# Kernel optimization log

Hardware: AMD Instinct MI355X
Metric: run time of the kernel (lower is better)

## Reference

```python
import jax, jax.numpy as jnp
import numpy as np

NEG = -1e30  # log-space 'zero'


def setup_inputs() -> dict:
    B, T, C, L = 64, 2000, 128, 200  # C = num_classes + 1, blank = C - 1
    key = jax.random.key(0)
    k1, k2, k3 = jax.random.split(key, 3)
    y_pred = jax.random.normal(k1, (B, T, C), dtype=jnp.float32)
    label_lengths = jax.random.randint(k2, (B,), L // 2, L + 1).astype(jnp.int32)
    labels = jax.random.randint(k3, (B, L), 0, C - 1).astype(jnp.int32)  # never blank
    # pad with -1 beyond each label length (matches tf sparse construction)
    valid = jnp.arange(L)[None, :] < label_lengths[:, None]
    y_true = jnp.where(valid, labels, -1).astype(jnp.int32)
    # train_step fills input_lengths with the full time dimension
    input_lengths = jnp.full((B,), T, dtype=jnp.int32)
    return {"y_pred": y_pred, "y_true": y_true,
            "input_lengths": input_lengths, "label_lengths": label_lengths}


def _lse3(a, b, c):
    m = jnp.maximum(jnp.maximum(a, b), c)
    return m + jnp.log(jnp.exp(a - m) + jnp.exp(b - m) + jnp.exp(c - m))


def _ctc_loss(y_pred, y_true, input_lengths, label_lengths):
    B, T, C = y_pred.shape
    blank = C - 1  # blank_index=-1 in tf.nn.ctc_loss
    logp = jax.nn.log_softmax(y_pred, axis=-1)          # [B,T,C]
    Lmax = y_true.shape[1]
    S = 2 * Lmax + 1                                     # extended label lattice
    lab = jnp.where(y_true < 0, 0, y_true).astype(jnp.int32)
    # extended labels: blank, l0, blank, l1, ..., blank
    ext = jnp.full((B, S), blank, jnp.int32).at[:, 1::2].set(lab)
    ext_m2 = jnp.concatenate([jnp.full((B, 2), blank, jnp.int32), ext[:, :-2]], axis=1)
    can_skip = (ext != blank) & (ext != ext_m2)          # [B,S]

    logp_t = jnp.transpose(logp, (1, 0, 2))              # [T,B,C]
    lp0 = jnp.take_along_axis(logp_t[0], ext, axis=1)    # [B,S]
    alpha = jnp.full((B, S), NEG, jnp.float32)
    alpha = alpha.at[:, 0].set(lp0[:, 0]).at[:, 1].set(lp0[:, 1])

    def step(alpha, xs):
        lp, t = xs                                       # lp: [B,C]
        lp_ext = jnp.take_along_axis(lp, ext, axis=1)    # [B,S]
        a1 = jnp.concatenate([jnp.full((B, 1), NEG, jnp.float32), alpha[:, :-1]], axis=1)
        a2 = jnp.concatenate([jnp.full((B, 2), NEG, jnp.float32), alpha[:, :-2]], axis=1)
        a2 = jnp.where(can_skip, a2, NEG)
        new = _lse3(alpha, a1, a2) + lp_ext
        new = jnp.where(t < input_lengths[:, None], new, alpha)  # freeze past seq end
        return new, None

    alpha, _ = jax.lax.scan(step, alpha, (logp_t[1:], jnp.arange(1, T)))

    s_end = (2 * label_lengths).astype(jnp.int32)        # [B]
    a_last = jnp.take_along_axis(alpha, s_end[:, None], axis=1)[:, 0]
    a_prev = jnp.take_along_axis(alpha, jnp.maximum(s_end - 1, 0)[:, None], axis=1)[:, 0]
    m = jnp.maximum(a_last, a_prev)
    ll = m + jnp.log(jnp.exp(a_last - m) + jnp.exp(a_prev - m))
    return -ll                                           # per-example loss [B]


def reference(y_pred, y_true, input_lengths, label_lengths):
    return _ctc_loss(y_pred, y_true, input_lengths, label_lengths)
```

## Files before the change

kernel.cpp:

```cpp
#include <hip/hip_runtime.h>
#include <hip/hip_fp16.h>


#define LOG2E 1.44269504088896340736f
#define LN2F  0.69314718055994530942f

namespace {

constexpr int Bc = 64, Tc = 2000, Cc = 128, Lmaxc = 200;
constexpr int NPAIR = Tc / 2;
constexpr int PAIRB = 1024;
constexpr int BLANKB = 8192;
constexpr size_t SB = (size_t)NPAIR * PAIRB + BLANKB;
constexpr int CHP = 16;
constexpr int CHB = CHP * PAIRB;

typedef const __attribute__((address_space(1))) void* gas_ptr;
typedef __attribute__((address_space(3))) void* las_ptr;

__device__ __forceinline__ float dpp_shr1_f(float x) {
  return __int_as_float(
      __builtin_amdgcn_update_dpp(0, __float_as_int(x), 0x138, 0xF, 0xF, true));
}
__device__ __forceinline__ int dpp_shr1_i(int x) {
  return __builtin_amdgcn_update_dpp(0, x, 0x138, 0xF, 0xF, true);
}
template <int CTRL>
__device__ __forceinline__ float dpp_add(float v) {
  return v + __int_as_float(
      __builtin_amdgcn_update_dpp(0, __float_as_int(v), CTRL, 0xF, 0xF, true));
}
__device__ __forceinline__ float wave_sum_bcast(float v) {
  v = dpp_add<0x111>(v);
  v = dpp_add<0x112>(v);
  v = dpp_add<0x114>(v);
  v = dpp_add<0x118>(v);
  v = dpp_add<0x142>(v);
  v = dpp_add<0x143>(v);
  return __int_as_float(__builtin_amdgcn_readlane(__float_as_int(v), 63));
}

__global__ __launch_bounds__(256) void pack_kernel(
    const float* __restrict__ y, const int* __restrict__ y_true,
    char* __restrict__ W) {
  const int b = blockIdx.y;
  const int wv = threadIdx.x >> 6, lane = threadIdx.x & 63;
  const int t = blockIdx.x * 4 + wv;
  const int* labs = y_true + b * Lmaxc;
  int base = 4 * lane;
  if (base > Lmaxc - 4) base = Lmaxc - 4;
  const int4 L = *(const int4*)(labs + base);
  auto fix = [&](int v, int idx) {
    int r = (idx > Lmaxc - 1) ? L.w : v;
    return r < 0 ? 0 : r;
  };
  const int c0 = fix(L.x, 4 * lane), c1 = fix(L.y, 4 * lane + 1);
  const int c2 = fix(L.z, 4 * lane + 2), c3 = fix(L.w, 4 * lane + 3);
  const float2 yy = *(const float2*)(y + ((size_t)b * Tc + t) * Cc + 2 * lane);
  float e0 = exp2f(fminf(yy.x * LOG2E, 50.f));
  float e1 = exp2f(fminf(yy.y * LOG2E, 50.f));
  const float rs = 1.0f / wave_sum_bcast(e0 + e1);
  unsigned q2 = __builtin_bit_cast(unsigned, __floats2half2_rn(e0 * rs, e1 * rs));
  unsigned g0 = (unsigned)__builtin_amdgcn_ds_bpermute((c0 >> 1) << 2, (int)q2);
  unsigned g1 = (unsigned)__builtin_amdgcn_ds_bpermute((c1 >> 1) << 2, (int)q2);
  unsigned g2 = (unsigned)__builtin_amdgcn_ds_bpermute((c2 >> 1) << 2, (int)q2);
  unsigned g3 = (unsigned)__builtin_amdgcn_ds_bpermute((c3 >> 1) << 2, (int)q2);
  unsigned h0 = (c0 & 1) ? (g0 >> 16) : (g0 & 0xFFFFu);
  unsigned h1 = (c1 & 1) ? (g1 >> 16) : (g1 & 0xFFFFu);
  unsigned h2 = (c2 & 1) ? (g2 >> 16) : (g2 & 0xFFFFu);
  unsigned h3 = (c3 & 1) ? (g3 >> 16) : (g3 & 0xFFFFu);
  if (t > 0) {
    char* Wb = W + (size_t)b * SB;
    const int pr = (t - 1) >> 1, sl = 1 - (t & 1);
    *(uint2*)(Wb + pr * PAIRB + lane * 16 + sl * 8) =
        make_uint2(h0 | (h1 << 16), h2 | (h3 << 16));
    if (lane == 63)
      *(float*)(Wb + (size_t)NPAIR * PAIRB + (size_t)(t - 1) * 4) = e1 * rs;
  }
}

__global__ __launch_bounds__(64) void ctc_alpha_kernel(
    const float* __restrict__ y, const char* __restrict__ W,
    const int* __restrict__ y_true, const int* __restrict__ in_len,
    const int* __restrict__ lab_len, float* __restrict__ out) {
  __shared__ __align__(16) char bufs[2][CHB];
  __shared__ __align__(16) float blk_s[BLANKB / 4];
  const int b = blockIdx.x, lane = threadIdx.x;
  int len = in_len[b];
  len = len < 1 ? 1 : (len > Tc ? Tc : len);
  const int ll = lab_len[b];
  const int* labs = y_true + b * Lmaxc;
  auto labc = [&](int l) -> int {
    int lc = l < 0 ? 0 : (l > Lmaxc - 1 ? Lmaxc - 1 : l);
    int c = labs[lc];
    return c < 0 ? 0 : c;
  };
  const int c0i = labc(4 * lane), c1i = labc(4 * lane + 1);
  const int c2i = labc(4 * lane + 2), c3i = labc(4 * lane + 3);
  const int cm1 = labc(4 * lane - 1), cm2 = labc(4 * lane - 2);
  const float sk0 = (4 * lane >= 1 && c0i != cm1) ? 1.f : 0.f;
  const float sk1 = (c1i != c0i) ? 1.f : 0.f;
  const float sk2 = (c2i != c1i) ? 1.f : 0.f;
  const float sk3 = (c3i != c2i) ? 1.f : 0.f;
  const float skH = (lane >= 1 && cm1 != cm2) ? 1.f : 0.f;
  const int lane16 = lane * 16;

  const char* Wb = W + (size_t)b * SB;
  auto load_pairs = [&](int bi, int k) {
#pragma unroll
    for (int j = 0; j < CHP; ++j) {
      unsigned off = (unsigned)(CHP * k + j) * PAIRB + lane16;
      __builtin_amdgcn_global_load_lds((gas_ptr)(Wb + off),
                                       (las_ptr)(&bufs[bi][j * PAIRB]), 16, 0, 0);
    }
  };
  auto load_blanks = [&]() {
#pragma unroll
    for (int j = 0; j < 8; ++j)
      __builtin_amdgcn_global_load_lds(
          (gas_ptr)(Wb + NPAIR * PAIRB + j * 1024 + lane16),
          (las_ptr)((char*)blk_s + j * 1024), 16, 0, 0);
  };

  float a0 = 0.f, a1 = 0.f, a2 = 0.f, a3 = 0.f;
  float a4 = 0.f, a5 = 0.f, a6 = 0.f, a7 = 0.f;
  int E = 0;
  {
    const float* y0 = y + (size_t)b * Tc * Cc + 2 * lane;
    float e0 = exp2f(fminf(y0[0] * LOG2E, 50.f));
    float e1 = exp2f(fminf(y0[1] * LOG2E, 50.f));
    const float rs = 1.0f / wave_sum_bcast(e0 + e1);
    int l0 = labs[0];
    l0 = l0 < 0 ? 0 : l0;
    float ev = (l0 & 1) ? e1 : e0;
    float q0 = __int_as_float(__builtin_amdgcn_readlane(__float_as_int(ev), l0 >> 1)) * rs;
    float qb = __int_as_float(__builtin_amdgcn_readlane(__float_as_int(e1), 63)) * rs;
    if (lane == 0) { a0 = qb; a1 = q0; }
  }
  float s7d = dpp_shr1_f(a7), s6d = dpp_shr1_f(a6), s5d = dpp_shr1_f(a5);
  int epd = 0;
  float corr = (lane == 0) ? 0.f : 1.f;

  auto round2 = [&](uint4 rw, float2 bl, bool renorm) {
    float2 aLo = __half22float2(*(__half2*)&rw.x);
    float2 aHi = __half22float2(*(__half2*)&rw.y);
    float2 bLo = __half22float2(*(__half2*)&rw.z);
    float2 bHi = __half22float2(*(__half2*)&rw.w);
    const float qbA = bl.x, qbB = bl.y;
    const float qhA = dpp_shr1_f(aHi.y);
    const float w7 = s7d * corr, w6 = s6d * corr, w5 = s5d * corr;
    const float hA = (w7 + w6 + skH * w5) * qhA;
    float n0 = (a0 + w7) * qbA;
    float n1 = (a1 + a0 + sk0 * w7) * aLo.x;
    float n2 = (a2 + a1) * qbA;
    float n3 = (a3 + a2 + sk1 * a1) * aLo.y;
    float n4 = (a4 + a3) * qbA;
    float n5 = (a5 + a4 + sk2 * a3) * aHi.x;
    float n6 = (a6 + a5) * qbA;
    float n7 = (a7 + a6 + sk3 * a5) * aHi.y;
    a0 = (n0 + hA) * qbB;
    a1 = (n1 + n0 + sk0 * hA) * bLo.x;
    a2 = (n2 + n1) * qbB;
    a3 = (n3 + n2 + sk1 * n1) * bLo.y;
    a4 = (n4 + n3) * qbB;
    a5 = (n5 + n4 + sk2 * n3) * bHi.x;
    a6 = (n6 + n5) * qbB;
    a7 = (n7 + n6 + sk3 * n5) * bHi.y;
    if (renorm) {
      float mx = fmaxf(fmaxf(fmaxf(a0, a1), fmaxf(a2, a3)),
                       fmaxf(fmaxf(a4, a5), fmaxf(a6, a7)));
      unsigned bits = __float_as_uint(mx);
      bool z = (bits == 0u);
      int e = (int)(bits >> 23) - 127;
      float f = __uint_as_float((254u - (bits >> 23)) << 23);
      f = z ? 1.0f : f;
      a0 *= f; a1 *= f; a2 *= f; a3 *= f;
      a4 *= f; a5 *= f; a6 *= f; a7 *= f;
      E = z ? epd : (E + e);
    }
    s7d = dpp_shr1_f(a7);
    s6d = dpp_shr1_f(a6);
    s5d = dpp_shr1_f(a5);
    if (renorm) {
      epd = dpp_shr1_i(E);
      int de = epd - E;
      de = de < -126 ? -126 : (de > 60 ? 60 : de);
      corr = __int_as_float((de + 127) << 23);
      corr = (lane == 0) ? 0.0f : corr;
    }
  };

  const int R = (len - 1) >> 1;
  const int leftover = (len - 1) & 1;
  const int PRtot = R + leftover;
  const int NCg = (PRtot + CHP - 1) / CHP;
  const int cfull = R / CHP;

  load_blanks();
  if (NCg > 0) load_pairs(0, 0);
  __builtin_amdgcn_s_waitcnt(0x0f70);
  if (NCg > 1) load_pairs(1, 1);

  uint4 raw[2];
  float2 blkp[2];
  if (NCg > 0) {
    raw[0] = *(const uint4*)(&bufs[0][0 * PAIRB] + lane16);
    blkp[0] = *(const float2*)(blk_s + 0);
    raw[1] = *(const uint4*)(&bufs[0][1 * PAIRB] + lane16);
    blkp[1] = *(const float2*)(blk_s + 2);
  }

  for (int c = 0; c < cfull; ++c) {
    const char* base = &bufs[c & 1][0];
    const char* nbase = &bufs[(c + 1) & 1][0];
    const float* pb = blk_s + c * 32;
#pragma unroll
    for (int rr = 0; rr < 16; ++rr) {
      const int p = rr & 1;
      uint4 rw = raw[p];
      float2 bl = blkp[p];
      if (rr < 14) {
        raw[p] = *(const uint4*)(base + (rr + 2) * PAIRB + lane16);
        blkp[p] = *(const float2*)(pb + (rr + 2) * 2);
      } else {
        if (rr == 14) __builtin_amdgcn_s_waitcnt(0x0f70);
        raw[p] = *(const uint4*)(nbase + (rr - 14) * PAIRB + lane16);
        blkp[p] = *(const float2*)(pb + 32 + (rr - 14) * 2);
      }
      round2(rw, bl, (rr & 3) == 3);
    }
    if (c + 2 < NCg) load_pairs(c & 1, c + 2);
  }

  __builtin_amdgcn_s_waitcnt(0x0f70);
  {
    const char* tb = &bufs[cfull & 1][0];
    const float* pbT = blk_s + cfull * 32;
    const int rem = R - cfull * CHP;
    for (int r = 0; r < rem; ++r) {
      uint4 rw = *(const uint4*)(tb + r * PAIRB + lane16);
      float2 bl = *(const float2*)(pbT + 2 * r);
      round2(rw, bl, (r & 3) == 3);
    }
    if (leftover) {
      uint4 rw = *(const uint4*)(tb + rem * PAIRB + lane16);
      float blA = *(pbT + 2 * rem);
      float2 flo = __half22float2(*(__half2*)&rw.x);
      float2 fhi = __half22float2(*(__half2*)&rw.y);
      float s7 = dpp_shr1_f(a7);
      int ep = dpp_shr1_i(E);
      int de = ep - E;
      de = de < -126 ? -126 : (de > 60 ? 60 : de);
      float c2 = __int_as_float((de + 127) << 23);
      c2 = (lane == 0) ? 0.0f : c2;
      float w7 = s7 * c2;
      float n0 = (a0 + w7) * blA;
      float n1 = (a1 + a0 + sk0 * w7) * flo.x;
      float n2 = (a2 + a1) * blA;
      float n3 = (a3 + a2 + sk1 * a1) * flo.y;
      float n4 = (a4 + a3) * blA;
      float n5 = (a5 + a4 + sk2 * a3) * fhi.x;
      float n6 = (a6 + a5) * blA;
      float n7 = (a7 + a6 + sk3 * a5) * fhi.y;
      a0 = n0; a1 = n1; a2 = n2; a3 = n3;
      a4 = n4; a5 = n5; a6 = n6; a7 = n7;
    }
  }

  int sE = 2 * ll;
  int sP = sE - 1 < 0 ? 0 : sE - 1;
  int laneA = sE >> 3, jA = sE & 7;
  int laneB = sP >> 3, jB = sP & 7;
  float va = a0;
  if (jA == 1) va = a1;
  if (jA == 2) va = a2;
  if (jA == 3) va = a3;
  if (jA == 4) va = a4;
  if (jA == 5) va = a5;
  if (jA == 6) va = a6;
  if (jA == 7) va = a7;
  float vb = a0;
  if (jB == 1) vb = a1;
  if (jB == 2) vb = a2;
  if (jB == 3) vb = a3;
  if (jB == 4) vb = a4;
  if (jB == 5) vb = a5;
  if (jB == 6) vb = a6;
  if (jB == 7) vb = a7;
  float aA = __int_as_float(__builtin_amdgcn_ds_bpermute(laneA << 2, __float_as_int(va)));
  float aB = __int_as_float(__builtin_amdgcn_ds_bpermute(laneB << 2, __float_as_int(vb)));
  int EA = __builtin_amdgcn_ds_bpermute(laneA << 2, E);
  int EB = __builtin_amdgcn_ds_bpermute(laneB << 2, E);
  if (lane == 0) {
    float l1 = (aA > 0.0f) ? (float)EA + log2f(aA) : -1e30f;
    float l2 = (aB > 0.0f) ? (float)EB + log2f(aB) : -1e30f;
    float mm = fmaxf(l1, l2);
    float v = mm + log2f(exp2f(l1 - mm) + exp2f(l2 - mm));
    out[b] = -v * LN2F;
  }
}

}

extern "C" void kernel_launch(void* const* d_in, const int* in_sizes, int n_in,
                              void* d_out, int out_size, void* d_ws, size_t ws_size,
                              hipStream_t stream) {
  const float* y = (const float*)d_in[0];
  const int* yt = (const int*)d_in[1];
  const int* il = (const int*)d_in[2];
  const int* lb = (const int*)d_in[3];
  float* out = (float*)d_out;
  char* W = (char*)d_ws;

  hipLaunchKernelGGL(pack_kernel, dim3(Tc / 4, Bc), dim3(256), 0, stream, y, yt, W);
  hipLaunchKernelGGL(ctc_alpha_kernel, dim3(Bc), dim3(64), 0, stream,
                     y, W, yt, il, lb, out);
}
```

Measured before the change: 257.7 us.

## Fuse pack and alpha kernels with producer-consumer watermark flags

Merges the packing kernel and the CTC alpha recursion into one launch. The first 64 blocks pack softmax probabilities per batch row and publish a progress watermark with release atomics, while the other 64 blocks run the recursion and spin on that watermark before streaming each chunk into LDS. The aim is to overlap packing with the serial recursion and drop the separate launch and the full pack pass that sat before it. In exchange, the pack work now runs on only 64 blocks, a memset is added, and correctness relies on producers and consumers being co-resident; the spin loop is bounded, so a missing producer could lead to stale reads.

New measurement: 498.0 us. +93.3%, slower.

```diff
diff --git a/kernel.cpp b/kernel.cpp
--- a/kernel.cpp
+++ b/kernel.cpp
@@ -10,8 +10,9 @@
 constexpr int Bc = 64, Tc = 2000, Cc = 128, Lmaxc = 200;
 constexpr int NPAIR = Tc / 2;
 constexpr int PAIRB = 1024;
-constexpr int BLANKB = 8192;
+constexpr int BLANKB = 8064;
 constexpr size_t SB = (size_t)NPAIR * PAIRB + BLANKB;
+constexpr size_t FLAGS_OFF = (size_t)Bc * SB;
 constexpr int CHP = 16;
 constexpr int CHB = CHP * PAIRB;
 
@@ -40,52 +41,69 @@
   return __int_as_float(__builtin_amdgcn_readlane(__float_as_int(v), 63));
 }
 
-__global__ __launch_bounds__(256) void pack_kernel(
-    const float* __restrict__ y, const int* __restrict__ y_true,
-    char* __restrict__ W) {
-  const int b = blockIdx.y;
-  const int wv = threadIdx.x >> 6, lane = threadIdx.x & 63;
-  const int t = blockIdx.x * 4 + wv;
-  const int* labs = y_true + b * Lmaxc;
-  int base = 4 * lane;
-  if (base > Lmaxc - 4) base = Lmaxc - 4;
-  const int4 L = *(const int4*)(labs + base);
-  auto fix = [&](int v, int idx) {
-    int r = (idx > Lmaxc - 1) ? L.w : v;
-    return r < 0 ? 0 : r;
-  };
-  const int c0 = fix(L.x, 4 * lane), c1 = fix(L.y, 4 * lane + 1);
-  const int c2 = fix(L.z, 4 * lane + 2), c3 = fix(L.w, 4 * lane + 3);
-  const float2 yy = *(const float2*)(y + ((size_t)b * Tc + t) * Cc + 2 * lane);
-  float e0 = exp2f(fminf(yy.x * LOG2E, 50.f));
-  float e1 = exp2f(fminf(yy.y * LOG2E, 50.f));
-  const float rs = 1.0f / wave_sum_bcast(e0 + e1);
-  unsigned q2 = __builtin_bit_cast(unsigned, __floats2half2_rn(e0 * rs, e1 * rs));
-  unsigned g0 = (unsigned)__builtin_amdgcn_ds_bpermute((c0 >> 1) << 2, (int)q2);
-  unsigned g1 = (unsigned)__builtin_amdgcn_ds_bpermute((c1 >> 1) << 2, (int)q2);
-  unsigned g2 = (unsigned)__builtin_amdgcn_ds_bpermute((c2 >> 1) << 2, (int)q2);
-  unsigned g3 = (unsigned)__builtin_amdgcn_ds_bpermute((c3 >> 1) << 2, (int)q2);
-  unsigned h0 = (c0 & 1) ? (g0 >> 16) : (g0 & 0xFFFFu);
-  unsigned h1 = (c1 & 1) ? (g1 >> 16) : (g1 & 0xFFFFu);
-  unsigned h2 = (c2 & 1) ? (g2 >> 16) : (g2 & 0xFFFFu);
-  unsigned h3 = (c3 & 1) ? (g3 >> 16) : (g3 & 0xFFFFu);
-  if (t > 0) {
-    char* Wb = W + (size_t)b * SB;
-    const int pr = (t - 1) >> 1, sl = 1 - (t & 1);
-    *(uint2*)(Wb + pr * PAIRB + lane * 16 + sl * 8) =
-        make_uint2(h0 | (h1 << 16), h2 | (h3 << 16));
-    if (lane == 63)
-      *(float*)(Wb + (size_t)NPAIR * PAIRB + (size_t)(t - 1) * 4) = e1 * rs;
-  }
-}
-
-__global__ __launch_bounds__(64) void ctc_alpha_kernel(
-    const float* __restrict__ y, const char* __restrict__ W,
+__global__ __launch_bounds__(256, 1) void ctc_fused_kernel(
+    const float* __restrict__ y, char* __restrict__ W,
     const int* __restrict__ y_true, const int* __restrict__ in_len,
     const int* __restrict__ lab_len, float* __restrict__ out) {
   __shared__ __align__(16) char bufs[2][CHB];
-  __shared__ __align__(16) float blk_s[BLANKB / 4];
-  const int b = blockIdx.x, lane = threadIdx.x;
+  __shared__ __align__(16) float blk_s[2048];
+
+  if (blockIdx.x < Bc) {
+    const int b = blockIdx.x;
+    const int wv = threadIdx.x >> 6, lane = threadIdx.x & 63;
+    const int* labs = y_true + b * Lmaxc;
+    int base = 4 * lane;
+    if (base > Lmaxc - 4) base = Lmaxc - 4;
+    const int4 L = *(const int4*)(labs + base);
+    auto fix = [&](int v, int idx) {
+      int r = (idx > Lmaxc - 1) ? L.w : v;
+      return r < 0 ? 0 : r;
+    };
+    const int c0 = fix(L.x, 4 * lane), c1 = fix(L.y, 4 * lane + 1);
+    const int c2 = fix(L.z, 4 * lane + 2), c3 = fix(L.w, 4 * lane + 3);
+    char* Wb = W + (size_t)b * SB;
+    int* wmp = (int*)(W + FLAGS_OFF) + b;
+    const float* yrow = y + (size_t)b * Tc * Cc + 2 * lane;
+
+    for (int p = 0; p < 32; ++p) {
+      const int t0 = p * 64 + wv * 16;
+#pragma unroll 4
+      for (int i = 0; i < 16; ++i) {
+        const int t = t0 + i;
+        if (t >= 1 && t < Tc) {
+          const float2 yy = *(const float2*)(yrow + (size_t)t * Cc);
+          float e0 = exp2f(fminf(yy.x * LOG2E, 50.f));
+          float e1 = exp2f(fminf(yy.y * LOG2E, 50.f));
+          const float rs = 1.0f / wave_sum_bcast(e0 + e1);
+          unsigned q2 =
+              __builtin_bit_cast(unsigned, __floats2half2_rn(e0 * rs, e1 * rs));
+          unsigned g0 = (unsigned)__builtin_amdgcn_ds_bpermute((c0 >> 1) << 2, (int)q2);
+          unsigned g1 = (unsigned)__builtin_amdgcn_ds_bpermute((c1 >> 1) << 2, (int)q2);
+          unsigned g2 = (unsigned)__builtin_amdgcn_ds_bpermute((c2 >> 1) << 2, (int)q2);
+          unsigned g3 = (unsigned)__builtin_amdgcn_ds_bpermute((c3 >> 1) << 2, (int)q2);
+          unsigned h0 = (c0 & 1) ? (g0 >> 16) : (g0 & 0xFFFFu);
+          unsigned h1 = (c1 & 1) ? (g1 >> 16) : (g1 & 0xFFFFu);
+          unsigned h2 = (c2 & 1) ? (g2 >> 16) : (g2 & 0xFFFFu);
+          unsigned h3 = (c3 & 1) ? (g3 >> 16) : (g3 & 0xFFFFu);
+          const int pr = (t - 1) >> 1, sl = 1 - (t & 1);
+          *(uint2*)(Wb + pr * PAIRB + lane * 16 + sl * 8) =
+              make_uint2(h0 | (h1 << 16), h2 | (h3 << 16));
+          if (lane == 63)
+            *(float*)(Wb + (size_t)NPAIR * PAIRB + (size_t)(t - 1) * 4) = e1 * rs;
+        }
+      }
+      __syncthreads();
+      if (threadIdx.x == 0 && ((p > 0 && (p & 3) == 0) || p == 31)) {
+        int v = 64 * (p + 1) - 1;
+        if (v > Tc - 1) v = Tc - 1;
+        __hip_atomic_store(wmp, v, __ATOMIC_RELEASE, __HIP_MEMORY_SCOPE_AGENT);
+      }
+    }
+    return;
+  }
+
+  if (threadIdx.x >= 64) return;
+  const int b = blockIdx.x - Bc, lane = threadIdx.x;
   int len = in_len[b];
   len = len < 1 ? 1 : (len > Tc ? Tc : len);
   const int ll = lab_len[b];
@@ -106,6 +124,14 @@
   const int lane16 = lane * 16;
 
   const char* Wb = W + (size_t)b * SB;
+  int* wmp = (int*)(W + FLAGS_OFF) + b;
+  auto wait_wm = [&](int need) {
+    for (int k = 0; k < (1 << 19); ++k) {
+      if (__hip_atomic_load(wmp, __ATOMIC_ACQUIRE, __HIP_MEMORY_SCOPE_AGENT) >= need)
+        break;
+      __builtin_amdgcn_s_sleep(2);
+    }
+  };
   auto load_pairs = [&](int bi, int k) {
 #pragma unroll
     for (int j = 0; j < CHP; ++j) {
@@ -114,12 +140,10 @@
                                        (las_ptr)(&bufs[bi][j * PAIRB]), 16, 0, 0);
     }
   };
-  auto load_blanks = [&]() {
-#pragma unroll
-    for (int j = 0; j < 8; ++j)
-      __builtin_amdgcn_global_load_lds(
-          (gas_ptr)(Wb + NPAIR * PAIRB + j * 1024 + lane16),
-          (las_ptr)((char*)blk_s + j * 1024), 16, 0, 0);
+  auto load_blank_region = [&](int r) {
+    __builtin_amdgcn_global_load_lds(
+        (gas_ptr)(Wb + NPAIR * PAIRB + r * 1024 + lane16),
+        (las_ptr)((char*)blk_s + r * 1024), 16, 0, 0);
   };
 
   float a0 = 0.f, a1 = 0.f, a2 = 0.f, a3 = 0.f;
@@ -196,7 +220,11 @@
   const int NCg = (PRtot + CHP - 1) / CHP;
   const int cfull = R / CHP;
 
-  load_blanks();
+  {
+    int need0 = 256 > Tc - 1 ? Tc - 1 : 256;
+    wait_wm(need0);
+  }
+  load_blank_region(0);
   if (NCg > 0) load_pairs(0, 0);
   __builtin_amdgcn_s_waitcnt(0x0f70);
   if (NCg > 1) load_pairs(1, 1);
@@ -229,7 +257,16 @@
       }
       round2(rw, bl, (rr & 3) == 3);
     }
-    if (c + 2 < NCg) load_pairs(c & 1, c + 2);
+    if (c + 2 < NCg) {
+      if (((c + 2) & 7) == 0) {
+        const int r = (c + 2) >> 3;
+        int need = 256 * (r + 1);
+        if (need > Tc - 1) need = Tc - 1;
+        wait_wm(need);
+        load_blank_region(r);
+      }
+      load_pairs(c & 1, c + 2);
+    }
   }
 
   __builtin_amdgcn_s_waitcnt(0x0f70);
@@ -312,7 +349,7 @@
   float* out = (float*)d_out;
   char* W = (char*)d_ws;
 
-  hipLaunchKernelGGL(pack_kernel, dim3(Tc / 4, Bc), dim3(256), 0, stream, y, yt, W);
-  hipLaunchKernelGGL(ctc_alpha_kernel, dim3(Bc), dim3(64), 0, stream,
+  hipMemsetAsync(W + FLAGS_OFF, 0, Bc * sizeof(int), stream);
+  hipLaunchKernelGGL(ctc_fused_kernel, dim3(2 * Bc), dim3(256), 0, stream,
                      y, W, yt, il, lb, out);
 }
```

## Fuse softmax packing into the alpha kernel with producer/consumer waves

Applied to the files above, without the earlier changes.

Merges the pack kernel and the alpha-recursion kernel into one 256-thread block per batch item. Three producer waves compute softmax-normalised half-precision label probabilities for the next 32-timestep chunk straight into double-buffered LDS. Meanwhile wave 0 runs the serial recurrence on the current chunk, with a block barrier between chunks. This removes the global workspace round trip and the second launch. In exchange, each block's 64 waves-worth of y loads now sit on the critical path of only 64 CUs, and a barrier is added per chunk.

Result: slower. 410.0 us (+59.1%).

```diff
diff --git a/kernel.cpp b/kernel.cpp
--- a/kernel.cpp
+++ b/kernel.cpp
@@ -8,15 +8,9 @@
 namespace {
 
 constexpr int Bc = 64, Tc = 2000, Cc = 128, Lmaxc = 200;
-constexpr int NPAIR = Tc / 2;
 constexpr int PAIRB = 1024;
-constexpr int BLANKB = 8192;
-constexpr size_t SB = (size_t)NPAIR * PAIRB + BLANKB;
 constexpr int CHP = 16;
 constexpr int CHB = CHP * PAIRB;
-
-typedef const __attribute__((address_space(1))) void* gas_ptr;
-typedef __attribute__((address_space(3))) void* las_ptr;
 
 __device__ __forceinline__ float dpp_shr1_f(float x) {
   return __int_as_float(
@@ -40,56 +34,67 @@
   return __int_as_float(__builtin_amdgcn_readlane(__float_as_int(v), 63));
 }
 
-__global__ __launch_bounds__(256) void pack_kernel(
+__global__ __launch_bounds__(256) void ctc_fused_kernel(
     const float* __restrict__ y, const int* __restrict__ y_true,
-    char* __restrict__ W) {
-  const int b = blockIdx.y;
+    const int* __restrict__ in_len, const int* __restrict__ lab_len,
+    float* __restrict__ out) {
+  __shared__ __align__(16) char bufs[2][CHB];
+  __shared__ __align__(16) float blkb[2][32];
+
+  const int b = blockIdx.x;
   const int wv = threadIdx.x >> 6, lane = threadIdx.x & 63;
-  const int t = blockIdx.x * 4 + wv;
-  const int* labs = y_true + b * Lmaxc;
-  int base = 4 * lane;
-  if (base > Lmaxc - 4) base = Lmaxc - 4;
-  const int4 L = *(const int4*)(labs + base);
-  auto fix = [&](int v, int idx) {
-    int r = (idx > Lmaxc - 1) ? L.w : v;
-    return r < 0 ? 0 : r;
-  };
-  const int c0 = fix(L.x, 4 * lane), c1 = fix(L.y, 4 * lane + 1);
-  const int c2 = fix(L.z, 4 * lane + 2), c3 = fix(L.w, 4 * lane + 3);
-  const float2 yy = *(const float2*)(y + ((size_t)b * Tc + t) * Cc + 2 * lane);
-  float e0 = exp2f(fminf(yy.x * LOG2E, 50.f));
-  float e1 = exp2f(fminf(yy.y * LOG2E, 50.f));
-  const float rs = 1.0f / wave_sum_bcast(e0 + e1);
-  unsigned q2 = __builtin_bit_cast(unsigned, __floats2half2_rn(e0 * rs, e1 * rs));
-  unsigned g0 = (unsigned)__builtin_amdgcn_ds_bpermute((c0 >> 1) << 2, (int)q2);
-  unsigned g1 = (unsigned)__builtin_amdgcn_ds_bpermute((c1 >> 1) << 2, (int)q2);
-  unsigned g2 = (unsigned)__builtin_amdgcn_ds_bpermute((c2 >> 1) << 2, (int)q2);
-  unsigned g3 = (unsigned)__builtin_amdgcn_ds_bpermute((c3 >> 1) << 2, (int)q2);
-  unsigned h0 = (c0 & 1) ? (g0 >> 16) : (g0 & 0xFFFFu);
-  unsigned h1 = (c1 & 1) ? (g1 >> 16) : (g1 & 0xFFFFu);
-  unsigned h2 = (c2 & 1) ? (g2 >> 16) : (g2 & 0xFFFFu);
-  unsigned h3 = (c3 & 1) ? (g3 >> 16) : (g3 & 0xFFFFu);
-  if (t > 0) {
-    char* Wb = W + (size_t)b * SB;
-    const int pr = (t - 1) >> 1, sl = 1 - (t & 1);
-    *(uint2*)(Wb + pr * PAIRB + lane * 16 + sl * 8) =
-        make_uint2(h0 | (h1 << 16), h2 | (h3 << 16));
-    if (lane == 63)
-      *(float*)(Wb + (size_t)NPAIR * PAIRB + (size_t)(t - 1) * 4) = e1 * rs;
-  }
-}
-
-__global__ __launch_bounds__(64) void ctc_alpha_kernel(
-    const float* __restrict__ y, const char* __restrict__ W,
-    const int* __restrict__ y_true, const int* __restrict__ in_len,
-    const int* __restrict__ lab_len, float* __restrict__ out) {
-  __shared__ __align__(16) char bufs[2][CHB];
-  __shared__ __align__(16) float blk_s[BLANKB / 4];
-  const int b = blockIdx.x, lane = threadIdx.x;
+  const int lane16 = lane * 16;
+
   int len = in_len[b];
   len = len < 1 ? 1 : (len > Tc ? Tc : len);
+  const int R = (len - 1) >> 1;
+  const int leftover = (len - 1) & 1;
+  const int PRtot = R + leftover;
+  const int NCg = (PRtot + CHP - 1) / CHP;
+  const int cfull = R / CHP;
+  const int* labs = y_true + b * Lmaxc;
+
+  int pbase = 4 * lane;
+  if (pbase > Lmaxc - 4) pbase = Lmaxc - 4;
+  const int4 Lw = *(const int4*)(labs + pbase);
+  auto fix = [&](int v, int idx) {
+    int r = (idx > Lmaxc - 1) ? Lw.w : v;
+    return r < 0 ? 0 : r;
+  };
+  const int c0 = fix(Lw.x, 4 * lane), c1 = fix(Lw.y, 4 * lane + 1);
+  const int c2 = fix(Lw.z, 4 * lane + 2), c3 = fix(Lw.w, 4 * lane + 3);
+  const float* yrow = y + (size_t)b * Tc * Cc + 2 * lane;
+
+  auto produce = [&](int kp) {
+    char* pbuf = &bufs[kp & 1][0];
+    float* bb = blkb[kp & 1];
+    int thi = 32 * kp + 32;
+    if (thi > Tc - 1) thi = Tc - 1;
+#pragma unroll 4
+    for (int t = 32 * kp + wv; t <= thi; t += 3) {
+      const float2 yy = *(const float2*)(yrow + (size_t)t * Cc);
+      float e0 = exp2f(fminf(yy.x * LOG2E, 50.f));
+      float e1 = exp2f(fminf(yy.y * LOG2E, 50.f));
+      const float rs = 1.0f / wave_sum_bcast(e0 + e1);
+      unsigned q2 =
+          __builtin_bit_cast(unsigned, __floats2half2_rn(e0 * rs, e1 * rs));
+      unsigned g0 = (unsigned)__builtin_amdgcn_ds_bpermute((c0 >> 1) << 2, (int)q2);
+      unsigned g1 = (unsigned)__builtin_amdgcn_ds_bpermute((c1 >> 1) << 2, (int)q2);
+      unsigned g2 = (unsigned)__builtin_amdgcn_ds_bpermute((c2 >> 1) << 2, (int)q2);
+      unsigned g3 = (unsigned)__builtin_amdgcn_ds_bpermute((c3 >> 1) << 2, (int)q2);
+      unsigned h0 = (c0 & 1) ? (g0 >> 16) : (g0 & 0xFFFFu);
+      unsigned h1 = (c1 & 1) ? (g1 >> 16) : (g1 & 0xFFFFu);
+      unsigned h2 = (c2 & 1) ? (g2 >> 16) : (g2 & 0xFFFFu);
+      unsigned h3 = (c3 & 1) ? (g3 >> 16) : (g3 & 0xFFFFu);
+      const int pq = ((t - 1) >> 1) - CHP * kp, sl = 1 - (t & 1);
+      *(uint2*)(pbuf + pq * PAIRB + lane16 + sl * 8) =
+          make_uint2(h0 | (h1 << 16), h2 | (h3 << 16));
+      if (lane == 63)
+        bb[(t - 1) - 32 * kp] = e1 * rs;
+    }
+  };
+
   const int ll = lab_len[b];
-  const int* labs = y_true + b * Lmaxc;
   auto labc = [&](int l) -> int {
     int lc = l < 0 ? 0 : (l > Lmaxc - 1 ? Lmaxc - 1 : l);
     int c = labs[lc];
@@ -103,29 +108,11 @@
   const float sk2 = (c2i != c1i) ? 1.f : 0.f;
   const float sk3 = (c3i != c2i) ? 1.f : 0.f;
   const float skH = (lane >= 1 && cm1 != cm2) ? 1.f : 0.f;
-  const int lane16 = lane * 16;
-
-  const char* Wb = W + (size_t)b * SB;
-  auto load_pairs = [&](int bi, int k) {
-#pragma unroll
-    for (int j = 0; j < CHP; ++j) {
-      unsigned off = (unsigned)(CHP * k + j) * PAIRB + lane16;
-      __builtin_amdgcn_global_load_lds((gas_ptr)(Wb + off),
-                                       (las_ptr)(&bufs[bi][j * PAIRB]), 16, 0, 0);
-    }
-  };
-  auto load_blanks = [&]() {
-#pragma unroll
-    for (int j = 0; j < 8; ++j)
-      __builtin_amdgcn_global_load_lds(
-          (gas_ptr)(Wb + NPAIR * PAIRB + j * 1024 + lane16),
-          (las_ptr)((char*)blk_s + j * 1024), 16, 0, 0);
-  };
 
   float a0 = 0.f, a1 = 0.f, a2 = 0.f, a3 = 0.f;
   float a4 = 0.f, a5 = 0.f, a6 = 0.f, a7 = 0.f;
   int E = 0;
-  {
+  if (wv == 0) {
     const float* y0 = y + (size_t)b * Tc * Cc + 2 * lane;
     float e0 = exp2f(fminf(y0[0] * LOG2E, 50.f));
     float e1 = exp2f(fminf(y0[1] * LOG2E, 50.f));
@@ -190,52 +177,48 @@
     }
   };
 
-  const int R = (len - 1) >> 1;
-  const int leftover = (len - 1) & 1;
-  const int PRtot = R + leftover;
-  const int NCg = (PRtot + CHP - 1) / CHP;
-  const int cfull = R / CHP;
-
-  load_blanks();
-  if (NCg > 0) load_pairs(0, 0);
-  __builtin_amdgcn_s_waitcnt(0x0f70);
-  if (NCg > 1) load_pairs(1, 1);
-
-  uint4 raw[2];
-  float2 blkp[2];
-  if (NCg > 0) {
-    raw[0] = *(const uint4*)(&bufs[0][0 * PAIRB] + lane16);
-    blkp[0] = *(const float2*)(blk_s + 0);
-    raw[1] = *(const uint4*)(&bufs[0][1 * PAIRB] + lane16);
-    blkp[1] = *(const float2*)(blk_s + 2);
+  auto consume = [&](int k) {
+    const char* cb = &bufs[k & 1][0];
+    const float* pb = blkb[k & 1];
+    uint4 rawA = *(const uint4*)(cb + 0 * PAIRB + lane16);
+    float2 blA = *(const float2*)(pb + 0);
+    uint4 rawB = *(const uint4*)(cb + 1 * PAIRB + lane16);
+    float2 blB = *(const float2*)(pb + 2);
+#pragma unroll
+    for (int h = 0; h < 8; ++h) {
+      uint4 ra = rawA;
+      float2 ba = blA;
+      if (h < 7) {
+        rawA = *(const uint4*)(cb + (2 * h + 2) * PAIRB + lane16);
+        blA = *(const float2*)(pb + (4 * h + 4));
+      }
+      round2(ra, ba, false);
+      uint4 rb = rawB;
+      float2 bb2 = blB;
+      if (h < 7) {
+        rawB = *(const uint4*)(cb + (2 * h + 3) * PAIRB + lane16);
+        blB = *(const float2*)(pb + (4 * h + 6));
+      }
+      round2(rb, bb2, (h & 1) == 1);
+    }
+  };
+
+  if (wv != 0 && NCg > 0) produce(0);
+  __syncthreads();
+  for (int k = 0; k < cfull; ++k) {
+    if (wv == 0) {
+      consume(k);
+    } else if (k + 1 < NCg) {
+      produce(k + 1);
+    }
+    __syncthreads();
   }
 
-  for (int c = 0; c < cfull; ++c) {
-    const char* base = &bufs[c & 1][0];
-    const char* nbase = &bufs[(c + 1) & 1][0];
-    const float* pb = blk_s + c * 32;
-#pragma unroll
-    for (int rr = 0; rr < 16; ++rr) {
-      const int p = rr & 1;
-      uint4 rw = raw[p];
-      float2 bl = blkp[p];
-      if (rr < 14) {
-        raw[p] = *(const uint4*)(base + (rr + 2) * PAIRB + lane16);
-        blkp[p] = *(const float2*)(pb + (rr + 2) * 2);
-      } else {
-        if (rr == 14) __builtin_amdgcn_s_waitcnt(0x0f70);
-        raw[p] = *(const uint4*)(nbase + (rr - 14) * PAIRB + lane16);
-        blkp[p] = *(const float2*)(pb + 32 + (rr - 14) * 2);
-      }
-      round2(rw, bl, (rr & 3) == 3);
-    }
-    if (c + 2 < NCg) load_pairs(c & 1, c + 2);
-  }
-
-  __builtin_amdgcn_s_waitcnt(0x0f70);
+  if (wv != 0) return;
+
   {
     const char* tb = &bufs[cfull & 1][0];
-    const float* pbT = blk_s + cfull * 32;
+    const float* pbT = blkb[cfull & 1];
     const int rem = R - cfull * CHP;
     for (int r = 0; r < rem; ++r) {
       uint4 rw = *(const uint4*)(tb + r * PAIRB + lane16);
@@ -251,9 +234,9 @@
       int ep = dpp_shr1_i(E);
       int de = ep - E;
       de = de < -126 ? -126 : (de > 60 ? 60 : de);
-      float c2 = __int_as_float((de + 127) << 23);
-      c2 = (lane == 0) ? 0.0f : c2;
-      float w7 = s7 * c2;
+      float c2v = __int_as_float((de + 127) << 23);
+      c2v = (lane == 0) ? 0.0f : c2v;
+      float w7 = s7 * c2v;
       float n0 = (a0 + w7) * blA;
       float n1 = (a1 + a0 + sk0 * w7) * flo.x;
       float n2 = (a2 + a1) * blA;
@@ -310,9 +293,8 @@
   const int* il = (const int*)d_in[2];
   const int* lb = (const int*)d_in[3];
   float* out = (float*)d_out;
-  char* W = (char*)d_ws;
-
-  hipLaunchKernelGGL(pack_kernel, dim3(Tc / 4, Bc), dim3(256), 0, stream, y, yt, W);
-  hipLaunchKernelGGL(ctc_alpha_kernel, dim3(Bc), dim3(64), 0, stream,
-                     y, W, yt, il, lb, out);
-}
+  (void)d_ws; (void)ws_size;
+
+  hipLaunchKernelGGL(ctc_fused_kernel, dim3(Bc), dim3(256), 0, stream,
+                     y, yt, il, lb, out);
+}
```
